# Optimization experiments

Hardware: AMD Instinct MI355X
Metric: run time of the kernel (lower is better)

## Reference

```python
import jax, jax.numpy as jnp
import numpy as np

N = 8192
D = 512


def setup_inputs() -> dict:
    key = jax.random.key(0)
    k_h, k_a, k_q, k_k, k_v = jax.random.split(key, 5)
    H = jax.random.normal(k_h, (N, D), dtype=jnp.float32)
    A = jax.random.uniform(k_a, (N, N), dtype=jnp.float32)
    W_Q = jax.random.uniform(k_q, (D, D), dtype=jnp.float32)
    W_K = jax.random.uniform(k_k, (D, D), dtype=jnp.float32)
    W_V = jax.random.uniform(k_v, (D, D), dtype=jnp.float32)
    return {"H": H, "A": A, "W_Q": W_Q, "W_K": W_K, "W_V": W_V}


def reference(H, A, W_Q, W_K, W_V):
    # Q = H @ W_Q, K = H @ W_K; scores = Q @ K^T  -> [N, N]
    scale = 1.0 / jnp.sqrt(jnp.asarray(H.shape[1], dtype=H.dtype))
    HQ = H @ W_Q                      # [N, D]
    HK = H @ W_K                      # [N, D]
    scores = jnp.einsum('nd,md->nm', HQ, HK)  # [N, N]
    scores = scores * A * scale       # elementwise adjacency mask + scale
    attn = jax.nn.softmax(scores, axis=1)
    return attn @ (H @ W_V)           # [N, D]
```

## Files before the change

### kernel.cpp

```cpp
#include <hip/hip_runtime.h>
#include <cmath>


typedef unsigned short u16;
typedef unsigned int   u32;
typedef float f32x4 __attribute__((ext_vector_type(4)));
typedef short s16x8 __attribute__((ext_vector_type(8)));

#define DEVI static __device__ __forceinline__

DEVI u16 f2bf(float x) { u32 u = __float_as_uint(x); u32 r = u + 0x7fffu + ((u >> 16) & 1u); return (u16)(r >> 16); }
DEVI float bf2f(u16 b) { return __uint_as_float((u32)b << 16); }

DEVI f32x4 mm_bf16(s16x8 a, s16x8 b, f32x4 c) {
  return __builtin_amdgcn_mfma_f32_16x16x32_bf16(a, b, c, 0, 0, 0);
}

DEVI uint4 scaleP(uint4 v, float f) {
  u32* w = (u32*)&v;
#pragma unroll
  for (int j = 0; j < 4; j++) {
    u32 lo = __float_as_uint(__uint_as_float(w[j] << 16) * f) + 0x8000u;
    u32 hi = __float_as_uint(__uint_as_float(w[j] & 0xffff0000u) * f) + 0x8000u;
    w[j] = __builtin_amdgcn_perm(hi, lo, 0x07060302);
  }
  return v;
}


__global__ void k_split(const float* __restrict__ X, u16* __restrict__ Xhi, u16* __restrict__ Xlo, int n4) {
  int i = blockIdx.x * 256 + threadIdx.x;
  if (i >= n4) return;
  float4 v = ((const float4*)X)[i];
  u16 h0 = f2bf(v.x), h1 = f2bf(v.y), h2 = f2bf(v.z), h3 = f2bf(v.w);
  u16 l0 = f2bf(v.x - bf2f(h0)), l1 = f2bf(v.y - bf2f(h1));
  u16 l2 = f2bf(v.z - bf2f(h2)), l3 = f2bf(v.w - bf2f(h3));
  ((uint2*)Xhi)[i] = make_uint2((u32)h0 | ((u32)h1 << 16), (u32)h2 | ((u32)h3 << 16));
  ((uint2*)Xlo)[i] = make_uint2((u32)l0 | ((u32)l1 << 16), (u32)l2 | ((u32)l3 << 16));
}

__global__ void k_prepW(const float* __restrict__ W0, const float* __restrict__ W1, const float* __restrict__ W2,
                        u16* __restrict__ Thi, u16* __restrict__ Tlo) {
  int idx = blockIdx.x * 256 + threadIdx.x;
  if (idx >= 3 * 512 * 512) return;
  int w = idx >> 18, n = (idx >> 9) & 511, k = idx & 511;
  const float* W = (w == 0) ? W0 : (w == 1) ? W1 : W2;
  float v = W[k * 512 + n];
  u16 h = f2bf(v);
  Thi[idx] = h;
  Tlo[idx] = f2bf(v - bf2f(h));
}

__global__ void k_transpose(const u16* __restrict__ in, u16* __restrict__ out, int R, int C) {
  __shared__ u16 t[64][72];
  const int rb = blockIdx.x * 64, cb = blockIdx.y * 64;
  const int r = threadIdx.x >> 2, c4 = (threadIdx.x & 3) * 16;
  const u16* src = in + (size_t)(rb + r) * C + cb + c4;
  *(uint4*)&t[r][c4] = *(const uint4*)src;
  *(uint4*)&t[r][c4 + 8] = *(const uint4*)(src + 8);
  __syncthreads();
  u16 v[16];
#pragma unroll
  for (int j = 0; j < 16; j++) v[j] = t[c4 + j][r];
  uint4 o0, o1;
  o0.x = v[0] | ((u32)v[1] << 16); o0.y = v[2] | ((u32)v[3] << 16);
  o0.z = v[4] | ((u32)v[5] << 16); o0.w = v[6] | ((u32)v[7] << 16);
  o1.x = v[8] | ((u32)v[9] << 16); o1.y = v[10] | ((u32)v[11] << 16);
  o1.z = v[12] | ((u32)v[13] << 16); o1.w = v[14] | ((u32)v[15] << 16);
  u16* dst = out + (size_t)(cb + r) * R + rb + c4;
  *(uint4*)dst = o0;
  *(uint4*)(dst + 8) = o1;
}


template<int EPI, int PASSES, int FUSEW, int KSPLIT>
__launch_bounds__(256, 4)
__global__ void gemm_bt(const u16* __restrict__ Ahi, const u16* __restrict__ Alo,
                        const u16* __restrict__ Bhi, const u16* __restrict__ Blo,
                        int M, int N, int K,
                        float* __restrict__ Cf, float* __restrict__ Cf1, float* __restrict__ Cf2,
                        u16* __restrict__ C0, u16* __restrict__ C1,
                        const float* __restrict__ Adj, float* __restrict__ mC, float* __restrict__ lC,
                        u16* __restrict__ Pout, const float* __restrict__ Fsc, float scale)
{
  constexpr int BUF = 128 * 40;
  constexpr int NBUF = (PASSES == 3) ? 4 : 3;
  __shared__ __align__(16) u16 lds[BUF * NBUF];

  u16* sAh = lds;
  u16* sAl = lds + BUF;
  u16* sBh = lds + ((PASSES == 3) ? 2 : 1) * BUF;
  u16* sBl = lds + ((PASSES == 3) ? 3 : 2) * BUF;

  const int tid = threadIdx.x, lane = tid & 63, wid = tid >> 6;
  const int wm = wid & 1, wn = wid >> 1;
  const int lr = lane & 15, lk = lane >> 4;
  const int mbase = blockIdx.x * 128;
  int nbase;
  const u16 *bhp = Bhi, *blp = Blo;
  u16 *c0 = C0, *c1 = C1;
  if constexpr (FUSEW) {
    const int w = blockIdx.y >> 2;
    nbase = (blockIdx.y & 3) * 128;
    bhp += (size_t)w * 262144;  blp += (size_t)w * 262144;
    c0  += (size_t)w * 4194304; c1  += (size_t)w * 4194304;
  } else {
    nbase = blockIdx.y * 128;
  }
  const int srow = tid >> 1, shalf = tid & 1;
  const size_t Ks = (size_t)K;

  int kbeg = 0, kend = K;
  if constexpr (KSPLIT > 1) {
    const int steps = K >> 5, bz = blockIdx.z;
    kbeg = ((steps * bz) / KSPLIT) << 5;
    kend = ((steps * (bz + 1)) / KSPLIT) << 5;
  }

  f32x4 acc[4][4] = {};

  for (int kt = kbeg; kt < kend; kt += 32) {
    const size_t aoff = (size_t)(mbase + srow) * Ks + kt + shalf * 16;
    const size_t boff = (size_t)(nbase + srow) * Ks + kt + shalf * 16;
    uint4 vah0 = *(const uint4*)(Ahi + aoff), vah1 = *(const uint4*)(Ahi + aoff + 8);
    uint4 vbh0 = *(const uint4*)(bhp + boff), vbh1 = *(const uint4*)(bhp + boff + 8);
    uint4 val0, val1, vbl0, vbl1;
    if constexpr (PASSES == 3) { val0 = *(const uint4*)(Alo + aoff); val1 = *(const uint4*)(Alo + aoff + 8); }
    vbl0 = *(const uint4*)(blp + boff); vbl1 = *(const uint4*)(blp + boff + 8);
    if constexpr (EPI == 3) {
      const float f = Fsc[((size_t)(kt >> 7) << 13) + mbase + srow];
      vah0 = scaleP(vah0, f); vah1 = scaleP(vah1, f);
    }
    __syncthreads();
    const int so = srow * 40 + shalf * 16;
    *(uint4*)(sAh + so) = vah0; *(uint4*)(sAh + so + 8) = vah1;
    *(uint4*)(sBh + so) = vbh0; *(uint4*)(sBh + so + 8) = vbh1;
    if constexpr (PASSES == 3) { *(uint4*)(sAl + so) = val0; *(uint4*)(sAl + so + 8) = val1; }
    *(uint4*)(sBl + so) = vbl0; *(uint4*)(sBl + so + 8) = vbl1;
    __syncthreads();

    s16x8 ah[4], bh[4], al[4], bl[4];
#pragma unroll
    for (int t = 0; t < 4; t++) {
      ah[t] = *(const s16x8*)(sAh + (wm * 64 + t * 16 + lr) * 40 + lk * 8);
      bh[t] = *(const s16x8*)(sBh + (wn * 64 + t * 16 + lr) * 40 + lk * 8);
      if constexpr (PASSES == 3) al[t] = *(const s16x8*)(sAl + (wm * 64 + t * 16 + lr) * 40 + lk * 8);
      bl[t] = *(const s16x8*)(sBl + (wn * 64 + t * 16 + lr) * 40 + lk * 8);
    }
#pragma unroll
    for (int mt = 0; mt < 4; mt++)
#pragma unroll
      for (int nt = 0; nt < 4; nt++) {
        acc[mt][nt] = mm_bf16(ah[mt], bh[nt], acc[mt][nt]);
        acc[mt][nt] = mm_bf16(ah[mt], bl[nt], acc[mt][nt]);
        if constexpr (PASSES == 3) acc[mt][nt] = mm_bf16(al[mt], bh[nt], acc[mt][nt]);
      }
  }

  if constexpr (EPI == 2) {
    __syncthreads();
    float* sred = (float*)lds;
    float* ssum = sred + 256;
    u16* pb = lds + 1024;
    float mfin[4];
#pragma unroll
    for (int nt = 0; nt < 4; nt++) {
      const int q_l = wn * 64 + nt * 16 + lr;
      const float* arow = Adj + (size_t)(nbase + q_l) * (size_t)M + mbase + wm * 64 + lk * 4;
      float4 a4[4];
#pragma unroll
      for (int mt = 0; mt < 4; mt++) a4[mt] = *(const float4*)(arow + mt * 16);
      float mx = -3.4e38f;
#pragma unroll
      for (int mt = 0; mt < 4; mt++)
#pragma unroll
        for (int r = 0; r < 4; r++) {
          float s = acc[mt][nt][r] * ((const float*)&a4[mt])[r] * scale;
          acc[mt][nt][r] = s;
          mx = fmaxf(mx, s);
        }
      mx = fmaxf(mx, __shfl_xor(mx, 16));
      mx = fmaxf(mx, __shfl_xor(mx, 32));
      if (lane < 16) sred[wm * 128 + wn * 64 + nt * 16 + lane] = mx;
    }
    __syncthreads();
#pragma unroll
    for (int nt = 0; nt < 4; nt++) {
      const int qi = wn * 64 + nt * 16 + lr;
      mfin[nt] = fmaxf(sred[qi], sred[128 + qi]);
    }
    if (wm == 0 && lane < 16) {
#pragma unroll
      for (int nt = 0; nt < 4; nt++)
        mC[(size_t)blockIdx.x * N + nbase + wn * 64 + nt * 16 + lane] = mfin[nt];
    }
#pragma unroll
    for (int nt = 0; nt < 4; nt++) {
      float sm = 0.f;
#pragma unroll
      for (int mt = 0; mt < 4; mt++)
#pragma unroll
        for (int r = 0; r < 4; r++) {
          float p = __expf(acc[mt][nt][r] - mfin[nt]);
          acc[mt][nt][r] = p;
          sm += p;
        }
      sm += __shfl_xor(sm, 16);
      sm += __shfl_xor(sm, 32);
      if (lane < 16) ssum[wm * 128 + wn * 64 + nt * 16 + lane] = sm;
    }
    __syncthreads();
    if (wm == 0 && lane < 16) {
#pragma unroll
      for (int nt = 0; nt < 4; nt++) {
        const int qi = wn * 64 + nt * 16 + lane;
        lC[(size_t)blockIdx.x * N + nbase + qi] = ssum[qi] + ssum[128 + qi];
      }
    }
#pragma unroll
    for (int nt = 0; nt < 4; nt++) {
      const int q_l = wn * 64 + nt * 16 + lr;
#pragma unroll
      for (int mt = 0; mt < 4; mt++) {
        const int kvo = wm * 64 + mt * 16 + lk * 4;
        u32 u0 = (u32)f2bf(acc[mt][nt][0]) | ((u32)f2bf(acc[mt][nt][1]) << 16);
        u32 u1 = (u32)f2bf(acc[mt][nt][2]) | ((u32)f2bf(acc[mt][nt][3]) << 16);
        *(uint2*)&pb[q_l * 136 + kvo] = make_uint2(u0, u1);
      }
    }
    __syncthreads();
    {
      u16* dst = Pout + (size_t)(nbase + srow) * (size_t)M + mbase + shalf * 64;
      const u16* srcp = &pb[srow * 136 + shalf * 64];
#pragma unroll
      for (int i = 0; i < 8; i++) ((uint4*)dst)[i] = ((const uint4*)srcp)[i];
    }
  } else {
    float* cfp = Cf;
    if constexpr (KSPLIT > 1) {
      if (blockIdx.z == 1) cfp = Cf1;
      else if (blockIdx.z == 2) cfp = Cf2;
    }
#pragma unroll
    for (int mt = 0; mt < 4; mt++)
#pragma unroll
      for (int nt = 0; nt < 4; nt++) {
        const int grow = mbase + wm * 64 + mt * 16 + lk * 4;
        const int gcol = nbase + wn * 64 + nt * 16 + lr;
#pragma unroll
        for (int r = 0; r < 4; r++) {
          float c = acc[mt][nt][r];
          size_t o = (size_t)(grow + r) * N + gcol;
          if constexpr (EPI == 0) {
            u16 h = f2bf(c);
            c0[o] = h;
            c1[o] = f2bf(c - bf2f(h));
          } else {
            cfp[o] = c;
          }
        }
      }
  }
}


__global__ void k_reduce(const float* __restrict__ mC, const float* __restrict__ lC, float* __restrict__ F,
                         int NQ, int NC) {
  const int q = blockIdx.x * 256 + threadIdx.x;
  if (q >= NQ) return;
  float mf = -3.4e38f;
  for (int c = 0; c < NC; c++) mf = fmaxf(mf, mC[(size_t)c * NQ + q]);
  float L = 0.f;
  for (int c = 0; c < NC; c++) L += lC[(size_t)c * NQ + q] * __expf(mC[(size_t)c * NQ + q] - mf);
  const float inv = 1.0f / L;
  for (int c = 0; c < NC; c++) F[(size_t)c * NQ + q] = __expf(mC[(size_t)c * NQ + q] - mf) * inv;
}

__global__ void k_sumout(float* __restrict__ out, const float* __restrict__ p1, const float* __restrict__ p2, int n4) {
  int i = blockIdx.x * 256 + threadIdx.x;
  if (i >= n4) return;
  float4 o = ((const float4*)out)[i];
  float4 a = ((const float4*)p1)[i];
  float4 b = ((const float4*)p2)[i];
  o.x += a.x + b.x; o.y += a.y + b.y; o.z += a.z + b.z; o.w += a.w + b.w;
  ((float4*)out)[i] = o;
}


extern "C" void kernel_launch(void* const* d_in, const int* in_sizes, int n_in,
                              void* d_out, int out_size, void* d_ws, size_t ws_size,
                              hipStream_t stream) {
  const float* H  = (const float*)d_in[0];
  const float* Aj = (const float*)d_in[1];
  const float* Wq = (const float*)d_in[2];
  const float* Wk = (const float*)d_in[3];
  const float* Wv = (const float*)d_in[4];
  float* out = (float*)d_out;
  const int NN = 8192, DD = 512;

  char* ws = (char*)d_ws;
  size_t off = 0;
  auto alloc = [&](size_t bytes) -> void* {
    void* p = ws + off;
    off += (bytes + 255) & ~(size_t)255;
    return p;
  };
  u16* Pbuf  = (u16*)alloc((size_t)NN * NN * 2);
  u16* Hhi   = (u16*)alloc((size_t)NN * DD * 2);
  u16* Hlo   = (u16*)alloc((size_t)NN * DD * 2);
  u16* WThi  = (u16*)alloc((size_t)3 * DD * DD * 2);
  u16* WTlo  = (u16*)alloc((size_t)3 * DD * DD * 2);
  u16* PRhi  = (u16*)alloc((size_t)3 * NN * DD * 2);
  u16* PRlo  = (u16*)alloc((size_t)3 * NN * DD * 2);
  u16* HVthi = (u16*)alloc((size_t)NN * DD * 2);
  u16* HVtlo = (u16*)alloc((size_t)NN * DD * 2);
  float* mC  = (float*)alloc((size_t)64 * NN * 4);
  float* lC  = (float*)alloc((size_t)64 * NN * 4);
  float* Ft  = (float*)alloc((size_t)64 * NN * 4);
  if (off > ws_size) return;

  u16* HQhi = PRhi;                 u16* HQlo = PRlo;
  u16* HKhi = PRhi + (size_t)NN*DD; u16* HKlo = PRlo + (size_t)NN*DD;
  u16* HVhi = PRhi + (size_t)2*NN*DD; u16* HVlo = PRlo + (size_t)2*NN*DD;

  float* part1 = (float*)Hhi;
  float* part2 = (float*)((char*)Hhi + (size_t)NN * DD * 4);

  const float scl = 1.0f / sqrtf((float)DD);

  k_split<<<4096, 256, 0, stream>>>(H, Hhi, Hlo, NN * DD / 4);
  k_prepW<<<3072, 256, 0, stream>>>(Wq, Wk, Wv, WThi, WTlo);

  dim3 gP(64, 12);
  gemm_bt<0, 3, 1, 1><<<gP, 256, 0, stream>>>(Hhi, Hlo, WThi, WTlo, NN, DD, DD,
                                              nullptr, nullptr, nullptr, PRhi, PRlo,
                                              nullptr, nullptr, nullptr, nullptr, nullptr, 0.f);

  dim3 gT(128, 8);
  k_transpose<<<gT, 256, 0, stream>>>(HVhi, HVthi, NN, DD);
  k_transpose<<<gT, 256, 0, stream>>>(HVlo, HVtlo, NN, DD);

  dim3 gS(64, 64);
  gemm_bt<2, 3, 0, 1><<<gS, 256, 0, stream>>>(HKhi, HKlo, HQhi, HQlo, NN, NN, DD,
                                              nullptr, nullptr, nullptr, nullptr, nullptr,
                                              Aj, mC, lC, Pbuf, nullptr, scl);

  k_reduce<<<32, 256, 0, stream>>>(mC, lC, Ft, NN, 64);

  dim3 gO(64, 4, 3);
  gemm_bt<3, 2, 0, 3><<<gO, 256, 0, stream>>>(Pbuf, nullptr, HVthi, HVtlo, NN, DD, NN,
                                              out, part1, part2, nullptr, nullptr,
                                              nullptr, nullptr, nullptr, nullptr, Ft, 0.f);

  k_sumout<<<4096, 256, 0, stream>>>(out, part1, part2, NN * DD / 4);
}
```

Before: 554.7 us.

## Add dedicated scores kernel with direct global-to-LDS double-buffered pipeline

Replaces the generic templated GEMM for the scores/softmax stage with a specialised kernel. Its tiles are loaded with global_load_lds straight into LDS and double-buffered. Loads for the next K-step are interleaved between MFMA phases, with s_setprio raising priority around the MFMA loops. The goal is to hide global memory latency and cut register staging in the dominant N×N stage, at the cost of more LDS per block (64KB, launch bound 2), more barriers, and hardcoded sizes. The epilogue is unchanged, and the old EPI==2 path is removed from the generic template.

```diff
diff --git a/kernel.cpp b/kernel.cpp
--- a/kernel.cpp
+++ b/kernel.cpp
@@ -14,6 +14,11 @@
 
 DEVI f32x4 mm_bf16(s16x8 a, s16x8 b, f32x4 c) {
   return __builtin_amdgcn_mfma_f32_16x16x32_bf16(a, b, c, 0, 0, 0);
+}
+
+DEVI void gll16(const u16* g, u16* l) {
+  __builtin_amdgcn_global_load_lds((const __attribute__((address_space(1))) void*)g,
+                                   (__attribute__((address_space(3))) void*)l, 16, 0, 0);
 }
 
 DEVI uint4 scaleP(uint4 v, float f) {
@@ -73,6 +78,173 @@
 }
 
 
+__launch_bounds__(256, 2)
+__global__ void k_scores(const u16* __restrict__ Ahi, const u16* __restrict__ Alo,
+                         const u16* __restrict__ Bhi, const u16* __restrict__ Blo,
+                         const float* __restrict__ Adj, float* __restrict__ mC,
+                         float* __restrict__ lC, u16* __restrict__ Pout, float scale)
+{
+  constexpr int NN = 8192, KK = 512;
+  __shared__ __align__(16) u16 lds[32768];
+
+  const int tid = threadIdx.x, lane = tid & 63, wid = tid >> 6;
+  const int wm = wid & 1, wn = wid >> 1;
+  const int lr = lane & 15, lk = lane >> 4;
+  const int mbase = blockIdx.x * 128, nbase = blockIdx.y * 128;
+  const int srow = tid >> 2, scol = tid & 3;
+
+  auto stage = [&](const u16* __restrict__ g, int gr0, u16* lp0, int kt) {
+    gll16(g + (size_t)(gr0 + srow) * KK + kt + scol * 8, lp0 + tid * 8);
+  };
+
+  u16* b0 = lds;
+  u16* b1 = lds + 16384;
+
+  stage(Ahi, mbase, b0, 0);          stage(Ahi, mbase + 64, b0 + 2048, 0);
+  stage(Alo, mbase, b0 + 4096, 0);   stage(Alo, mbase + 64, b0 + 6144, 0);
+  stage(Bhi, nbase, b0 + 8192, 0);   stage(Bhi, nbase + 64, b0 + 10240, 0);
+  stage(Blo, nbase, b0 + 12288, 0);  stage(Blo, nbase + 64, b0 + 14336, 0);
+  asm volatile("s_waitcnt vmcnt(0)" ::: "memory");
+  __builtin_amdgcn_s_barrier();
+
+  f32x4 acc[4][4] = {};
+
+  for (int t = 0; t < 16; ++t) {
+    u16* cb = (t & 1) ? b1 : b0;
+    u16* nb = (t & 1) ? b0 : b1;
+    const int nkt = (t + 1) << 5;
+    const bool more = (t < 15);
+    s16x8 ah[4], bh[4], al[4], bl[4];
+
+#pragma unroll
+    for (int x = 0; x < 4; x++) {
+      ah[x] = *(const s16x8*)(cb + (wm * 64 + x * 16 + lr) * 32 + lk * 8);
+      bh[x] = *(const s16x8*)(cb + 8192 + (wn * 64 + x * 16 + lr) * 32 + lk * 8);
+    }
+    if (more) {
+      stage(Ahi, mbase, nb, nkt);        stage(Ahi, mbase + 64, nb + 2048, nkt);
+      stage(Alo, mbase, nb + 4096, nkt); stage(Alo, mbase + 64, nb + 6144, nkt);
+    }
+    __builtin_amdgcn_s_barrier();
+    __builtin_amdgcn_s_setprio(1);
+#pragma unroll
+    for (int mt = 0; mt < 4; mt++)
+#pragma unroll
+      for (int nt = 0; nt < 4; nt++) acc[mt][nt] = mm_bf16(ah[mt], bh[nt], acc[mt][nt]);
+    __builtin_amdgcn_s_setprio(0);
+    __builtin_amdgcn_s_barrier();
+
+#pragma unroll
+    for (int x = 0; x < 4; x++)
+      bl[x] = *(const s16x8*)(cb + 12288 + (wn * 64 + x * 16 + lr) * 32 + lk * 8);
+    if (more) {
+      stage(Bhi, nbase, nb + 8192, nkt);  stage(Bhi, nbase + 64, nb + 10240, nkt);
+      stage(Blo, nbase, nb + 12288, nkt); stage(Blo, nbase + 64, nb + 14336, nkt);
+    }
+    __builtin_amdgcn_s_barrier();
+    __builtin_amdgcn_s_setprio(1);
+#pragma unroll
+    for (int mt = 0; mt < 4; mt++)
+#pragma unroll
+      for (int nt = 0; nt < 4; nt++) acc[mt][nt] = mm_bf16(ah[mt], bl[nt], acc[mt][nt]);
+    __builtin_amdgcn_s_setprio(0);
+    __builtin_amdgcn_s_barrier();
+
+#pragma unroll
+    for (int x = 0; x < 4; x++)
+      al[x] = *(const s16x8*)(cb + 4096 + (wm * 64 + x * 16 + lr) * 32 + lk * 8);
+    __builtin_amdgcn_s_barrier();
+    __builtin_amdgcn_s_setprio(1);
+#pragma unroll
+    for (int mt = 0; mt < 4; mt++)
+#pragma unroll
+      for (int nt = 0; nt < 4; nt++) acc[mt][nt] = mm_bf16(al[mt], bh[nt], acc[mt][nt]);
+    __builtin_amdgcn_s_setprio(0);
+    asm volatile("s_waitcnt vmcnt(0)" ::: "memory");
+    __builtin_amdgcn_s_barrier();
+  }
+
+  __syncthreads();
+  float* sred = (float*)lds;
+  float* ssum = sred + 256;
+  u16* pb = lds + 1024;
+  float mfin[4];
+#pragma unroll
+  for (int nt = 0; nt < 4; nt++) {
+    const int q_l = wn * 64 + nt * 16 + lr;
+    const float* arow = Adj + (size_t)(nbase + q_l) * (size_t)NN + mbase + wm * 64 + lk * 4;
+    float4 a4[4];
+#pragma unroll
+    for (int mt = 0; mt < 4; mt++) a4[mt] = *(const float4*)(arow + mt * 16);
+    float mx = -3.4e38f;
+#pragma unroll
+    for (int mt = 0; mt < 4; mt++)
+#pragma unroll
+      for (int r = 0; r < 4; r++) {
+        float s = acc[mt][nt][r] * ((const float*)&a4[mt])[r] * scale;
+        acc[mt][nt][r] = s;
+        mx = fmaxf(mx, s);
+      }
+    mx = fmaxf(mx, __shfl_xor(mx, 16));
+    mx = fmaxf(mx, __shfl_xor(mx, 32));
+    if (lane < 16) sred[wm * 128 + wn * 64 + nt * 16 + lane] = mx;
+  }
+  __syncthreads();
+#pragma unroll
+  for (int nt = 0; nt < 4; nt++) {
+    const int qi = wn * 64 + nt * 16 + lr;
+    mfin[nt] = fmaxf(sred[qi], sred[128 + qi]);
+  }
+  if (wm == 0 && lane < 16) {
+#pragma unroll
+    for (int nt = 0; nt < 4; nt++)
+      mC[(size_t)blockIdx.x * NN + nbase + wn * 64 + nt * 16 + lane] = mfin[nt];
+  }
+#pragma unroll
+  for (int nt = 0; nt < 4; nt++) {
+    float sm = 0.f;
+#pragma unroll
+    for (int mt = 0; mt < 4; mt++)
+#pragma unroll
+      for (int r = 0; r < 4; r++) {
+        float p = __expf(acc[mt][nt][r] - mfin[nt]);
+        acc[mt][nt][r] = p;
+        sm += p;
+      }
+    sm += __shfl_xor(sm, 16);
+    sm += __shfl_xor(sm, 32);
+    if (lane < 16) ssum[wm * 128 + wn * 64 + nt * 16 + lane] = sm;
+  }
+  __syncthreads();
+  if (wm == 0 && lane < 16) {
+#pragma unroll
+    for (int nt = 0; nt < 4; nt++) {
+      const int qi = wn * 64 + nt * 16 + lane;
+      lC[(size_t)blockIdx.x * NN + nbase + qi] = ssum[qi] + ssum[128 + qi];
+    }
+  }
+#pragma unroll
+  for (int nt = 0; nt < 4; nt++) {
+    const int q_l = wn * 64 + nt * 16 + lr;
+#pragma unroll
+    for (int mt = 0; mt < 4; mt++) {
+      const int kvo = wm * 64 + mt * 16 + lk * 4;
+      u32 u0 = (u32)f2bf(acc[mt][nt][0]) | ((u32)f2bf(acc[mt][nt][1]) << 16);
+      u32 u1 = (u32)f2bf(acc[mt][nt][2]) | ((u32)f2bf(acc[mt][nt][3]) << 16);
+      *(uint2*)&pb[q_l * 136 + kvo] = make_uint2(u0, u1);
+    }
+  }
+  __syncthreads();
+  {
+    const int prow = tid >> 1, phalf = tid & 1;
+    u16* dst = Pout + (size_t)(nbase + prow) * (size_t)NN + mbase + phalf * 64;
+    const u16* srcp = &pb[prow * 136 + phalf * 64];
+#pragma unroll
+    for (int i = 0; i < 8; i++) ((uint4*)dst)[i] = ((const uint4*)srcp)[i];
+  }
+}
+
+
 template<int EPI, int PASSES, int FUSEW, int KSPLIT>
 __launch_bounds__(256, 4)
 __global__ void gemm_bt(const u16* __restrict__ Ahi, const u16* __restrict__ Alo,
@@ -80,8 +252,7 @@
                         int M, int N, int K,
                         float* __restrict__ Cf, float* __restrict__ Cf1, float* __restrict__ Cf2,
                         u16* __restrict__ C0, u16* __restrict__ C1,
-                        const float* __restrict__ Adj, float* __restrict__ mC, float* __restrict__ lC,
-                        u16* __restrict__ Pout, const float* __restrict__ Fsc, float scale)
+                        const float* __restrict__ Fsc)
 {
   constexpr int BUF = 128 * 40;
   constexpr int NBUF = (PASSES == 3) ? 4 : 3;
@@ -157,110 +328,30 @@
       }
   }
 
-  if constexpr (EPI == 2) {
-    __syncthreads();
-    float* sred = (float*)lds;
-    float* ssum = sred + 256;
-    u16* pb = lds + 1024;
-    float mfin[4];
+  float* cfp = Cf;
+  if constexpr (KSPLIT > 1) {
+    if (blockIdx.z == 1) cfp = Cf1;
+    else if (blockIdx.z == 2) cfp = Cf2;
+  }
+#pragma unroll
+  for (int mt = 0; mt < 4; mt++)
 #pragma unroll
     for (int nt = 0; nt < 4; nt++) {
-      const int q_l = wn * 64 + nt * 16 + lr;
-      const float* arow = Adj + (size_t)(nbase + q_l) * (size_t)M + mbase + wm * 64 + lk * 4;
-      float4 a4[4];
-#pragma unroll
-      for (int mt = 0; mt < 4; mt++) a4[mt] = *(const float4*)(arow + mt * 16);
-      float mx = -3.4e38f;
-#pragma unroll
-      for (int mt = 0; mt < 4; mt++)
-#pragma unroll
-        for (int r = 0; r < 4; r++) {
-          float s = acc[mt][nt][r] * ((const float*)&a4[mt])[r] * scale;
-          acc[mt][nt][r] = s;
-          mx = fmaxf(mx, s);
-        }
-      mx = fmaxf(mx, __shfl_xor(mx, 16));
-      mx = fmaxf(mx, __shfl_xor(mx, 32));
-      if (lane < 16) sred[wm * 128 + wn * 64 + nt * 16 + lane] = mx;
-    }
-    __syncthreads();
-#pragma unroll
-    for (int nt = 0; nt < 4; nt++) {
-      const int qi = wn * 64 + nt * 16 + lr;
-      mfin[nt] = fmaxf(sred[qi], sred[128 + qi]);
-    }
-    if (wm == 0 && lane < 16) {
-#pragma unroll
-      for (int nt = 0; nt < 4; nt++)
-        mC[(size_t)blockIdx.x * N + nbase + wn * 64 + nt * 16 + lane] = mfin[nt];
-    }
-#pragma unroll
-    for (int nt = 0; nt < 4; nt++) {
-      float sm = 0.f;
-#pragma unroll
-      for (int mt = 0; mt < 4; mt++)
-#pragma unroll
-        for (int r = 0; r < 4; r++) {
-          float p = __expf(acc[mt][nt][r] - mfin[nt]);
-          acc[mt][nt][r] = p;
-          sm += p;
-        }
-      sm += __shfl_xor(sm, 16);
-      sm += __shfl_xor(sm, 32);
-      if (lane < 16) ssum[wm * 128 + wn * 64 + nt * 16 + lane] = sm;
-    }
-    __syncthreads();
-    if (wm == 0 && lane < 16) {
-#pragma unroll
-      for (int nt = 0; nt < 4; nt++) {
-        const int qi = wn * 64 + nt * 16 + lane;
-        lC[(size_t)blockIdx.x * N + nbase + qi] = ssum[qi] + ssum[128 + qi];
-      }
-    }
-#pragma unroll
-    for (int nt = 0; nt < 4; nt++) {
-      const int q_l = wn * 64 + nt * 16 + lr;
-#pragma unroll
-      for (int mt = 0; mt < 4; mt++) {
-        const int kvo = wm * 64 + mt * 16 + lk * 4;
-        u32 u0 = (u32)f2bf(acc[mt][nt][0]) | ((u32)f2bf(acc[mt][nt][1]) << 16);
-        u32 u1 = (u32)f2bf(acc[mt][nt][2]) | ((u32)f2bf(acc[mt][nt][3]) << 16);
-        *(uint2*)&pb[q_l * 136 + kvo] = make_uint2(u0, u1);
-      }
-    }
-    __syncthreads();
-    {
-      u16* dst = Pout + (size_t)(nbase + srow) * (size_t)M + mbase + shalf * 64;
-      const u16* srcp = &pb[srow * 136 + shalf * 64];
-#pragma unroll
-      for (int i = 0; i < 8; i++) ((uint4*)dst)[i] = ((const uint4*)srcp)[i];
-    }
-  } else {
-    float* cfp = Cf;
-    if constexpr (KSPLIT > 1) {
-      if (blockIdx.z == 1) cfp = Cf1;
-      else if (blockIdx.z == 2) cfp = Cf2;
-    }
-#pragma unroll
-    for (int mt = 0; mt < 4; mt++)
-#pragma unroll
-      for (int nt = 0; nt < 4; nt++) {
-        const int grow = mbase + wm * 64 + mt * 16 + lk * 4;
-        const int gcol = nbase + wn * 64 + nt * 16 + lr;
-#pragma unroll
-        for (int r = 0; r < 4; r++) {
-          float c = acc[mt][nt][r];
-          size_t o = (size_t)(grow + r) * N + gcol;
-          if constexpr (EPI == 0) {
-            u16 h = f2bf(c);
-            c0[o] = h;
-            c1[o] = f2bf(c - bf2f(h));
-          } else {
-            cfp[o] = c;
-          }
+      const int grow = mbase + wm * 64 + mt * 16 + lk * 4;
+      const int gcol = nbase + wn * 64 + nt * 16 + lr;
+#pragma unroll
+      for (int r = 0; r < 4; r++) {
+        float c = acc[mt][nt][r];
+        size_t o = (size_t)(grow + r) * N + gcol;
+        if constexpr (EPI == 0) {
+          u16 h = f2bf(c);
+          c0[o] = h;
+          c1[o] = f2bf(c - bf2f(h));
+        } else {
+          cfp[o] = c;
         }
       }
-  }
+    }
 }
 
 
@@ -333,24 +424,20 @@
 
   dim3 gP(64, 12);
   gemm_bt<0, 3, 1, 1><<<gP, 256, 0, stream>>>(Hhi, Hlo, WThi, WTlo, NN, DD, DD,
-                                              nullptr, nullptr, nullptr, PRhi, PRlo,
-                                              nullptr, nullptr, nullptr, nullptr, nullptr, 0.f);
+                                              nullptr, nullptr, nullptr, PRhi, PRlo, nullptr);
 
   dim3 gT(128, 8);
   k_transpose<<<gT, 256, 0, stream>>>(HVhi, HVthi, NN, DD);
   k_transpose<<<gT, 256, 0, stream>>>(HVlo, HVtlo, NN, DD);
 
   dim3 gS(64, 64);
-  gemm_bt<2, 3, 0, 1><<<gS, 256, 0, stream>>>(HKhi, HKlo, HQhi, HQlo, NN, NN, DD,
-                                              nullptr, nullptr, nullptr, nullptr, nullptr,
-                                              Aj, mC, lC, Pbuf, nullptr, scl);
+  k_scores<<<gS, 256, 0, stream>>>(HKhi, HKlo, HQhi, HQlo, Aj, mC, lC, Pbuf, scl);
 
   k_reduce<<<32, 256, 0, stream>>>(mC, lC, Ft, NN, 64);
 
   dim3 gO(64, 4, 3);
   gemm_bt<3, 2, 0, 3><<<gO, 256, 0, stream>>>(Pbuf, nullptr, HVthi, HVtlo, NN, DD, NN,
-                                              out, part1, part2, nullptr, nullptr,
-                                              nullptr, nullptr, nullptr, nullptr, Ft, 0.f);
+                                              out, part1, part2, nullptr, nullptr, Ft);
 
   k_sumout<<<4096, 256, 0, stream>>>(out, part1, part2, NN * DD / 4);
 }
```

Measured after the change: 562.1 us. No clear change (+1.3%).

## Add dedicated 256x256-tile scores kernel with direct-to-LDS loads and swizzled LDS

Applied to the files above, without the earlier changes.

Replaces the generic 128x128 gemm_bt scores path with a specialized k_scores kernel: 512 threads, 256x256 tiles, double-buffered LDS filled via global_load_lds, XOR-swizzled layout, and interleaved MFMA phases with setprio. Each wave now covers 128 kv columns, so per-chunk max/sum are written per half-block (c = blockIdx.x*2+wm), which keeps 64 chunks for k_reduce. The aim is more operand reuse per tile, fewer LDS bank conflicts, and load latency hidden behind MFMA work. In exchange it hardcodes N=8192 and D=512, and the larger per-thread accumulator set (8x4 f32x4) adds register pressure, which may limit occupancy.

```diff
diff --git a/kernel.cpp b/kernel.cpp
--- a/kernel.cpp
+++ b/kernel.cpp
@@ -14,6 +14,11 @@
 
 DEVI f32x4 mm_bf16(s16x8 a, s16x8 b, f32x4 c) {
   return __builtin_amdgcn_mfma_f32_16x16x32_bf16(a, b, c, 0, 0, 0);
+}
+
+DEVI void gll16(const u16* g, u16* l) {
+  __builtin_amdgcn_global_load_lds((const __attribute__((address_space(1))) void*)g,
+                                   (__attribute__((address_space(3))) void*)l, 16, 0, 0);
 }
 
 DEVI uint4 scaleP(uint4 v, float f) {
@@ -73,6 +78,182 @@
 }
 
 
+#define SC_MFMA2(m, a0, a1, al0, al1) \
+  _Pragma("unroll") for (int nt = 0; nt < 4; nt++) acc[(m)][nt]     = mm_bf16(a0,  bh[nt], acc[(m)][nt]);     \
+  _Pragma("unroll") for (int nt = 0; nt < 4; nt++) acc[(m) + 1][nt] = mm_bf16(a1,  bh[nt], acc[(m) + 1][nt]); \
+  _Pragma("unroll") for (int nt = 0; nt < 4; nt++) acc[(m)][nt]     = mm_bf16(a0,  bl[nt], acc[(m)][nt]);     \
+  _Pragma("unroll") for (int nt = 0; nt < 4; nt++) acc[(m) + 1][nt] = mm_bf16(a1,  bl[nt], acc[(m) + 1][nt]); \
+  _Pragma("unroll") for (int nt = 0; nt < 4; nt++) acc[(m)][nt]     = mm_bf16(al0, bh[nt], acc[(m)][nt]);     \
+  _Pragma("unroll") for (int nt = 0; nt < 4; nt++) acc[(m) + 1][nt] = mm_bf16(al1, bh[nt], acc[(m) + 1][nt]);
+
+__launch_bounds__(512, 2)
+__global__ void k_scores(const u16* __restrict__ Ahi, const u16* __restrict__ Alo,
+                         const u16* __restrict__ Bhi, const u16* __restrict__ Blo,
+                         const float* __restrict__ Adj, float* __restrict__ mC,
+                         float* __restrict__ lC, u16* __restrict__ Pout, float scale)
+{
+  constexpr int NN = 8192;
+  __shared__ __align__(16) u16 lds[65536];
+
+  const int tid = threadIdx.x, lane = tid & 63, wid = tid >> 6;
+  const int wm = wid >> 2, wn = wid & 3;
+  const int lr = lane & 15, lk = lane >> 4;
+  const int mbase = blockIdx.x * 256, nbase = blockIdx.y * 256;
+
+  const int rA = wm * 128 + lr;
+  const int rB = wn * 64 + lr;
+  const int ofsA = rA * 32 + (lk ^ ((rA >> 1) & 3)) * 8;
+  const int ofsB = 16384 + rB * 32 + (lk ^ ((rB >> 1) & 3)) * 8;
+
+  const int srow = tid >> 2;
+  const int scol = ((tid & 3) ^ ((tid >> 3) & 3)) * 8;
+
+  u16* const buf0 = lds;
+  u16* const buf1 = lds + 32768;
+
+  auto stage4 = [&](u16* nb, const u16* g0, const u16* g1, int grow0, int kt, int arr) {
+    u16* d0 = nb + arr * 8192;
+    const size_t base = (size_t)(grow0 + srow) * 512 + kt + scol;
+    gll16(g0 + base,         d0 + tid * 8);
+    gll16(g0 + base + 65536, d0 + 4096 + tid * 8);
+    gll16(g1 + base,         d0 + 8192 + tid * 8);
+    gll16(g1 + base + 65536, d0 + 12288 + tid * 8);
+  };
+
+  stage4(buf0, Ahi, Alo, mbase, 0, 0);
+  stage4(buf0, Bhi, Blo, nbase, 0, 2);
+  asm volatile("s_waitcnt vmcnt(0)" ::: "memory");
+  __builtin_amdgcn_s_barrier();
+
+  f32x4 acc[8][4] = {};
+
+  for (int t = 0; t < 16; ++t) {
+    u16* cur = (t & 1) ? buf1 : buf0;
+    u16* nxt = (t & 1) ? buf0 : buf1;
+    const int nkt = (t + 1) << 5;
+    const bool more = t < 15;
+    s16x8 bh[4], bl[4], a0, a1, al0, al1;
+
+#pragma unroll
+    for (int nt = 0; nt < 4; nt++) {
+      bh[nt] = *(const s16x8*)(cur + ofsB + nt * 512);
+      bl[nt] = *(const s16x8*)(cur + 8192 + ofsB + nt * 512);
+    }
+    a0  = *(const s16x8*)(cur + ofsA);
+    a1  = *(const s16x8*)(cur + ofsA + 512);
+    al0 = *(const s16x8*)(cur + 8192 + ofsA);
+    al1 = *(const s16x8*)(cur + 8192 + ofsA + 512);
+    if (more) stage4(nxt, Ahi, Alo, mbase, nkt, 0);
+    __builtin_amdgcn_s_barrier();
+    asm volatile("s_waitcnt lgkmcnt(0)" ::: "memory");
+    __builtin_amdgcn_sched_barrier(0);
+    __builtin_amdgcn_s_setprio(1);
+    SC_MFMA2(0, a0, a1, al0, al1)
+    __builtin_amdgcn_s_setprio(0);
+    __builtin_amdgcn_s_barrier();
+
+    a0  = *(const s16x8*)(cur + ofsA + 2 * 512);
+    a1  = *(const s16x8*)(cur + ofsA + 3 * 512);
+    al0 = *(const s16x8*)(cur + 8192 + ofsA + 2 * 512);
+    al1 = *(const s16x8*)(cur + 8192 + ofsA + 3 * 512);
+    if (more) stage4(nxt, Bhi, Blo, nbase, nkt, 2);
+    __builtin_amdgcn_s_barrier();
+    asm volatile("s_waitcnt lgkmcnt(0)" ::: "memory");
+    __builtin_amdgcn_sched_barrier(0);
+    __builtin_amdgcn_s_setprio(1);
+    SC_MFMA2(2, a0, a1, al0, al1)
+    __builtin_amdgcn_s_setprio(0);
+    __builtin_amdgcn_s_barrier();
+
+    a0  = *(const s16x8*)(cur + ofsA + 4 * 512);
+    a1  = *(const s16x8*)(cur + ofsA + 5 * 512);
+    al0 = *(const s16x8*)(cur + 8192 + ofsA + 4 * 512);
+    al1 = *(const s16x8*)(cur + 8192 + ofsA + 5 * 512);
+    __builtin_amdgcn_s_barrier();
+    asm volatile("s_waitcnt lgkmcnt(0)" ::: "memory");
+    __builtin_amdgcn_sched_barrier(0);
+    __builtin_amdgcn_s_setprio(1);
+    SC_MFMA2(4, a0, a1, al0, al1)
+    __builtin_amdgcn_s_setprio(0);
+    __builtin_amdgcn_s_barrier();
+
+    a0  = *(const s16x8*)(cur + ofsA + 6 * 512);
+    a1  = *(const s16x8*)(cur + ofsA + 7 * 512);
+    al0 = *(const s16x8*)(cur + 8192 + ofsA + 6 * 512);
+    al1 = *(const s16x8*)(cur + 8192 + ofsA + 7 * 512);
+    __builtin_amdgcn_s_barrier();
+    asm volatile("s_waitcnt lgkmcnt(0)" ::: "memory");
+    __builtin_amdgcn_sched_barrier(0);
+    __builtin_amdgcn_s_setprio(1);
+    SC_MFMA2(6, a0, a1, al0, al1)
+    __builtin_amdgcn_s_setprio(0);
+    asm volatile("s_waitcnt vmcnt(0)" ::: "memory");
+    __builtin_amdgcn_s_barrier();
+  }
+
+  const int c = blockIdx.x * 2 + wm;
+#pragma unroll
+  for (int nt = 0; nt < 4; nt++) {
+    const int q_l = wn * 64 + nt * 16 + lr;
+    const float* arow = Adj + (size_t)(nbase + q_l) * NN + mbase + wm * 128 + lk * 4;
+    float4 a4[8];
+#pragma unroll
+    for (int mt = 0; mt < 8; mt++) a4[mt] = *(const float4*)(arow + mt * 16);
+    float mx = -3.4e38f;
+#pragma unroll
+    for (int mt = 0; mt < 8; mt++)
+#pragma unroll
+      for (int r = 0; r < 4; r++) {
+        float s = acc[mt][nt][r] * ((const float*)&a4[mt])[r] * scale;
+        acc[mt][nt][r] = s;
+        mx = fmaxf(mx, s);
+      }
+    mx = fmaxf(mx, __shfl_xor(mx, 16));
+    mx = fmaxf(mx, __shfl_xor(mx, 32));
+    float sm = 0.f;
+#pragma unroll
+    for (int mt = 0; mt < 8; mt++)
+#pragma unroll
+      for (int r = 0; r < 4; r++) {
+        float p = __expf(acc[mt][nt][r] - mx);
+        acc[mt][nt][r] = p;
+        sm += p;
+      }
+    sm += __shfl_xor(sm, 16);
+    sm += __shfl_xor(sm, 32);
+    if (lane < 16) {
+      mC[(size_t)c * NN + nbase + wn * 64 + nt * 16 + lane] = mx;
+      lC[(size_t)c * NN + nbase + wn * 64 + nt * 16 + lane] = sm;
+    }
+  }
+
+  u16* pb = lds;
+#pragma unroll
+  for (int nt = 0; nt < 4; nt++) {
+    const int q_l = wn * 64 + nt * 16 + lr;
+    const int qsw = (q_l & 7) << 3;
+#pragma unroll
+    for (int mt = 0; mt < 8; mt++) {
+      const int kv = wm * 128 + mt * 16 + lk * 4;
+      u32 u0 = (u32)f2bf(acc[mt][nt][0]) | ((u32)f2bf(acc[mt][nt][1]) << 16);
+      u32 u1 = (u32)f2bf(acc[mt][nt][2]) | ((u32)f2bf(acc[mt][nt][3]) << 16);
+      *(uint2*)&pb[q_l * 256 + (kv ^ qsw)] = make_uint2(u0, u1);
+    }
+  }
+  __syncthreads();
+  {
+    const int q_r = tid >> 1, half = tid & 1;
+    const int qsw = (q_r & 7) << 3;
+    u16* dst = Pout + (size_t)(nbase + q_r) * NN + mbase + half * 128;
+#pragma unroll
+    for (int i = 0; i < 16; i++) {
+      const int kv8 = (half * 128 + i * 8) ^ qsw;
+      *(uint4*)(dst + i * 8) = *(const uint4*)&pb[q_r * 256 + kv8];
+    }
+  }
+}
+
+
 template<int EPI, int PASSES, int FUSEW, int KSPLIT>
 __launch_bounds__(256, 4)
 __global__ void gemm_bt(const u16* __restrict__ Ahi, const u16* __restrict__ Alo,
@@ -80,8 +261,7 @@
                         int M, int N, int K,
                         float* __restrict__ Cf, float* __restrict__ Cf1, float* __restrict__ Cf2,
                         u16* __restrict__ C0, u16* __restrict__ C1,
-                        const float* __restrict__ Adj, float* __restrict__ mC, float* __restrict__ lC,
-                        u16* __restrict__ Pout, const float* __restrict__ Fsc, float scale)
+                        const float* __restrict__ Fsc)
 {
   constexpr int BUF = 128 * 40;
   constexpr int NBUF = (PASSES == 3) ? 4 : 3;
@@ -157,110 +337,30 @@
       }
   }
 
-  if constexpr (EPI == 2) {
-    __syncthreads();
-    float* sred = (float*)lds;
-    float* ssum = sred + 256;
-    u16* pb = lds + 1024;
-    float mfin[4];
+  float* cfp = Cf;
+  if constexpr (KSPLIT > 1) {
+    if (blockIdx.z == 1) cfp = Cf1;
+    else if (blockIdx.z == 2) cfp = Cf2;
+  }
+#pragma unroll
+  for (int mt = 0; mt < 4; mt++)
 #pragma unroll
     for (int nt = 0; nt < 4; nt++) {
-      const int q_l = wn * 64 + nt * 16 + lr;
-      const float* arow = Adj + (size_t)(nbase + q_l) * (size_t)M + mbase + wm * 64 + lk * 4;
-      float4 a4[4];
-#pragma unroll
-      for (int mt = 0; mt < 4; mt++) a4[mt] = *(const float4*)(arow + mt * 16);
-      float mx = -3.4e38f;
-#pragma unroll
-      for (int mt = 0; mt < 4; mt++)
-#pragma unroll
-        for (int r = 0; r < 4; r++) {
-          float s = acc[mt][nt][r] * ((const float*)&a4[mt])[r] * scale;
-          acc[mt][nt][r] = s;
-          mx = fmaxf(mx, s);
-        }
-      mx = fmaxf(mx, __shfl_xor(mx, 16));
-      mx = fmaxf(mx, __shfl_xor(mx, 32));
-      if (lane < 16) sred[wm * 128 + wn * 64 + nt * 16 + lane] = mx;
-    }
-    __syncthreads();
-#pragma unroll
-    for (int nt = 0; nt < 4; nt++) {
-      const int qi = wn * 64 + nt * 16 + lr;
-      mfin[nt] = fmaxf(sred[qi], sred[128 + qi]);
-    }
-    if (wm == 0 && lane < 16) {
-#pragma unroll
-      for (int nt = 0; nt < 4; nt++)
-        mC[(size_t)blockIdx.x * N + nbase + wn * 64 + nt * 16 + lane] = mfin[nt];
-    }
-#pragma unroll
-    for (int nt = 0; nt < 4; nt++) {
-      float sm = 0.f;
-#pragma unroll
-      for (int mt = 0; mt < 4; mt++)
-#pragma unroll
-        for (int r = 0; r < 4; r++) {
-          float p = __expf(acc[mt][nt][r] - mfin[nt]);
-          acc[mt][nt][r] = p;
-          sm += p;
-        }
-      sm += __shfl_xor(sm, 16);
-      sm += __shfl_xor(sm, 32);
-      if (lane < 16) ssum[wm * 128 + wn * 64 + nt * 16 + lane] = sm;
-    }
-    __syncthreads();
-    if (wm == 0 && lane < 16) {
-#pragma unroll
-      for (int nt = 0; nt < 4; nt++) {
-        const int qi = wn * 64 + nt * 16 + lane;
-        lC[(size_t)blockIdx.x * N + nbase + qi] = ssum[qi] + ssum[128 + qi];
-      }
-    }
-#pragma unroll
-    for (int nt = 0; nt < 4; nt++) {
-      const int q_l = wn * 64 + nt * 16 + lr;
-#pragma unroll
-      for (int mt = 0; mt < 4; mt++) {
-        const int kvo = wm * 64 + mt * 16 + lk * 4;
-        u32 u0 = (u32)f2bf(acc[mt][nt][0]) | ((u32)f2bf(acc[mt][nt][1]) << 16);
-        u32 u1 = (u32)f2bf(acc[mt][nt][2]) | ((u32)f2bf(acc[mt][nt][3]) << 16);
-        *(uint2*)&pb[q_l * 136 + kvo] = make_uint2(u0, u1);
-      }
-    }
-    __syncthreads();
-    {
-      u16* dst = Pout + (size_t)(nbase + srow) * (size_t)M + mbase + shalf * 64;
-      const u16* srcp = &pb[srow * 136 + shalf * 64];
-#pragma unroll
-      for (int i = 0; i < 8; i++) ((uint4*)dst)[i] = ((const uint4*)srcp)[i];
-    }
-  } else {
-    float* cfp = Cf;
-    if constexpr (KSPLIT > 1) {
-      if (blockIdx.z == 1) cfp = Cf1;
-      else if (blockIdx.z == 2) cfp = Cf2;
-    }
-#pragma unroll
-    for (int mt = 0; mt < 4; mt++)
-#pragma unroll
-      for (int nt = 0; nt < 4; nt++) {
-        const int grow = mbase + wm * 64 + mt * 16 + lk * 4;
-        const int gcol = nbase + wn * 64 + nt * 16 + lr;
-#pragma unroll
-        for (int r = 0; r < 4; r++) {
-          float c = acc[mt][nt][r];
-          size_t o = (size_t)(grow + r) * N + gcol;
-          if constexpr (EPI == 0) {
-            u16 h = f2bf(c);
-            c0[o] = h;
-            c1[o] = f2bf(c - bf2f(h));
-          } else {
-            cfp[o] = c;
-          }
+      const int grow = mbase + wm * 64 + mt * 16 + lk * 4;
+      const int gcol = nbase + wn * 64 + nt * 16 + lr;
+#pragma unroll
+      for (int r = 0; r < 4; r++) {
+        float c = acc[mt][nt][r];
+        size_t o = (size_t)(grow + r) * N + gcol;
+        if constexpr (EPI == 0) {
+          u16 h = f2bf(c);
+          c0[o] = h;
+          c1[o] = f2bf(c - bf2f(h));
+        } else {
+          cfp[o] = c;
         }
       }
-  }
+    }
 }
 
 
@@ -333,24 +433,20 @@
 
   dim3 gP(64, 12);
   gemm_bt<0, 3, 1, 1><<<gP, 256, 0, stream>>>(Hhi, Hlo, WThi, WTlo, NN, DD, DD,
-                                              nullptr, nullptr, nullptr, PRhi, PRlo,
-                                              nullptr, nullptr, nullptr, nullptr, nullptr, 0.f);
+                                              nullptr, nullptr, nullptr, PRhi, PRlo, nullptr);
 
   dim3 gT(128, 8);
   k_transpose<<<gT, 256, 0, stream>>>(HVhi, HVthi, NN, DD);
   k_transpose<<<gT, 256, 0, stream>>>(HVlo, HVtlo, NN, DD);
 
-  dim3 gS(64, 64);
-  gemm_bt<2, 3, 0, 1><<<gS, 256, 0, stream>>>(HKhi, HKlo, HQhi, HQlo, NN, NN, DD,
-                                              nullptr, nullptr, nullptr, nullptr, nullptr,
-                                              Aj, mC, lC, Pbuf, nullptr, scl);
+  dim3 gS(32, 32);
+  k_scores<<<gS, 512, 0, stream>>>(HKhi, HKlo, HQhi, HQlo, Aj, mC, lC, Pbuf, scl);
 
   k_reduce<<<32, 256, 0, stream>>>(mC, lC, Ft, NN, 64);
 
   dim3 gO(64, 4, 3);
   gemm_bt<3, 2, 0, 3><<<gO, 256, 0, stream>>>(Pbuf, nullptr, HVthi, HVtlo, NN, DD, NN,
-                                              out, part1, part2, nullptr, nullptr,
-                                              nullptr, nullptr, nullptr, nullptr, Ft, 0.f);
+                                              out, part1, part2, nullptr, nullptr, Ft);
 
   k_sumout<<<4096, 256, 0, stream>>>(out, part1, part2, NN * DD / 4);
 }
```

Result: slower. 578.2 us (+4.2%).
